# Optimization experiments

Hardware: AMD Instinct MI355X
Metric: run time of the kernel (lower is better)

## Reference

```python
import jax, jax.numpy as jnp
import numpy as np

B, N, D, H = 1, 4096, 1024, 16
K = D // H
ROPE_BASE = 10000.0


def _rope_cos_sin(n, k, base, dtype):
    # GPT-NeoX style rotary embedding: inv_freq over even dims, emb = cat(freqs, freqs)
    inv_freq = 1.0 / (base ** (jnp.arange(0, k, 2, dtype=jnp.float32) / k))  # [K/2]
    pos = jnp.arange(n, dtype=jnp.float32)
    freqs = pos[:, None] * inv_freq[None, :]              # [N, K/2]
    emb = jnp.concatenate([freqs, freqs], axis=-1)        # [N, K]
    return jnp.cos(emb).astype(dtype), jnp.sin(emb).astype(dtype)


def _rotate_half(x):
    x1, x2 = jnp.split(x, 2, axis=-1)
    return jnp.concatenate([-x2, x1], axis=-1)


def setup_inputs() -> dict:
    key = jax.random.key(0)
    kx, kq, ko = jax.random.split(key, 3)
    x = jax.random.normal(kx, (B, N, D), dtype=jnp.float32)
    # torch Linear weights: [out_features, in_features], y = x @ W^T
    w_qkv = jax.random.normal(kq, (3 * H * K, D), dtype=jnp.float32) / np.sqrt(D)
    w_out = jax.random.normal(ko, (D, D), dtype=jnp.float32) / np.sqrt(D)
    return {"x": x, "w_qkv": w_qkv, "w_out": w_out}


def reference(x, w_qkv, w_out):
    b, n, d = x.shape
    qkv = jnp.einsum('bnd,ed->bne', x, w_qkv).reshape(b, n, 3, H, K)
    q, k, v = qkv[:, :, 0], qkv[:, :, 1], qkv[:, :, 2]   # [B, N, H, K]
    cos, sin = _rope_cos_sin(n, K, ROPE_BASE, x.dtype)    # [N, K]
    cos = cos[None, :, None, :]
    sin = sin[None, :, None, :]
    q = q * cos + _rotate_half(q) * sin
    k = k * cos + _rotate_half(k) * sin
    # explicit O(N^2) score matrix, as in the original module
    scores = jnp.einsum('bnhk,bmhk->bnhm', q, k) / np.sqrt(K).astype(x.dtype)
    causal_mask = jnp.tril(jnp.ones((n, n), dtype=bool))  # [N, M]
    scores = jnp.where(causal_mask[None, :, None, :], scores, jnp.finfo(x.dtype).min)
    probs = jax.nn.softmax(scores, axis=-1)
    attn = jnp.einsum('bnhm,bmhk->bnhk', probs, v).reshape(b, n, d)
    return jnp.einsum('bnd,ed->bne', attn, w_out)
```

## Files before the change

### kernel.cpp

```cpp
#include <hip/hip_runtime.h>
#include <hip/hip_bf16.h>
#include <math.h>

#define N_SEQ 4096
#define DIM   1024
#define NHEAD 16
#define HDIM  64
#define E3    3072

typedef short bf16x8 __attribute__((ext_vector_type(8)));
typedef float f32x4  __attribute__((ext_vector_type(4)));
typedef unsigned int u32;

#if __has_builtin(__builtin_amdgcn_exp2f)
#define EXP2(x) __builtin_amdgcn_exp2f(x)
#else
#define EXP2(x) exp2f(x)
#endif

__device__ __forceinline__ float bf2f(unsigned short u) {
    union { unsigned int i; float f; } x; x.i = ((unsigned int)u) << 16; return x.f;
}
__device__ __forceinline__ unsigned short f2bf(float f) {
    union { float f; unsigned int i; } x; x.f = f;
    unsigned int r = x.i + 0x7FFF + ((x.i >> 16) & 1);
    return (unsigned short)(r >> 16);
}
__device__ __forceinline__ unsigned short f2bf_fast(float f) {
    union { float f; unsigned int i; } x; x.f = f;
    return (unsigned short)((x.i + 0x8000u) >> 16);
}
__device__ __forceinline__ f32x4 mfma16(bf16x8 a, bf16x8 b, f32x4 c) {
    return __builtin_amdgcn_mfma_f32_16x16x32_bf16(a, b, c, 0, 0, 0);
}
__device__ __forceinline__ void gload_lds16(const unsigned short* g, unsigned short* l) {
    __builtin_amdgcn_global_load_lds(
        (const __attribute__((address_space(1))) u32*)g,
        (__attribute__((address_space(3))) u32*)l, 16, 0, 0);
}

__device__ __forceinline__ int probe_isf32(const unsigned short* __restrict__ X) {
    __shared__ int cnt;
    if (threadIdx.x == 0) cnt = 0;
    __syncthreads();
    int bad = 0;
    for (int i = threadIdx.x; i < 4096; i += 256) {
        float v = bf2f(X[i]);
        if (!(fabsf(v) < 1e10f)) bad = 1;
    }
    if (bad) atomicAdd(&cnt, 1);
    __syncthreads();
    return cnt > 0;
}

__global__ __launch_bounds__(256)
void prep_kernel(const void* __restrict__ X, const void* __restrict__ Wq,
                 const void* __restrict__ Wo,
                 unsigned short* __restrict__ Xb, unsigned short* __restrict__ Wqb,
                 unsigned short* __restrict__ Wob,
                 float4* __restrict__ Rt,
                 int* __restrict__ flag)
{
    const int ti = blockIdx.x * blockDim.x + threadIdx.x;
    if (ti < N_SEQ * 16) {
        const int n = ti >> 4, f = ti & 15;
        const float i0 = powf(10000.f, -((float)f)        * (1.f/32.f));
        const float i1 = powf(10000.f, -((float)(f + 16)) * (1.f/32.f));
        float s0, c0, s1, c1;
        sincosf((float)n * i0, &s0, &c0);
        sincosf((float)n * i1, &s1, &c1);
        Rt[ti] = (float4){c0, c1, s0, s1};
    }

    const int isf32 = probe_isf32((const unsigned short*)X);
    if (blockIdx.x == 0 && threadIdx.x == 0) *flag = isf32;
    if (!isf32) return;

    const int nX4  = (N_SEQ * DIM) >> 2;
    const int nWq4 = (E3 * DIM) >> 2;
    const int nWo4 = (DIM * DIM) >> 2;
    const int total = nX4 + nWq4 + nWo4;
    const int stride = gridDim.x * blockDim.x;
    for (int i = blockIdx.x * blockDim.x + threadIdx.x; i < total; i += stride) {
        const float4* src; ushort4* dst; int j = i;
        if (j < nX4)                { src = (const float4*)X  + j;  dst = (ushort4*)Xb  + j; }
        else if ((j -= nX4) < nWq4) { src = (const float4*)Wq + j;  dst = (ushort4*)Wqb + j; }
        else { j -= nWq4;             src = (const float4*)Wo + j;  dst = (ushort4*)Wob + j; }
        float4 v = *src;
        ushort4 u;
        u.x = f2bf(v.x); u.y = f2bf(v.y); u.z = f2bf(v.z); u.w = f2bf(v.w);
        *dst = u;
    }
}

__global__ __launch_bounds__(256)
void qkv_mfma_kernel(const void* __restrict__ Xo, const unsigned short* __restrict__ Xc,
                     const void* __restrict__ Wo_, const unsigned short* __restrict__ Wc,
                     const int* __restrict__ flag,
                     const float4* __restrict__ Rt,
                     unsigned short* __restrict__ Qf,
                     unsigned short* __restrict__ Kf,
                     unsigned short* __restrict__ Vf)
{
    __shared__ __align__(16) unsigned short SMEM[4][4096];

    const int isf32 = *flag;
    const unsigned short* Xb = isf32 ? Xc : (const unsigned short*)Xo;
    const unsigned short* Wb = isf32 ? Wc : (const unsigned short*)Wo_;

    const int tid  = threadIdx.x;
    const int lane = tid & 63;
    const int wave = tid >> 6;
    const int wr = wave >> 1, wc = wave & 1;
    const int lm = lane & 15, q4 = lane >> 4;
    const int rbase = blockIdx.y * 128;
    const int cbase = blockIdx.x * 128;

    const int srow = wave * 16 + (lane >> 2);
    const int scol = (lane & 3) * 8;

    const unsigned short* xsrc = Xb + (size_t)(rbase + srow) * DIM + scol;
    const unsigned short* wsrc = Wb + (size_t)(cbase + srow) * DIM + scol;
    const int la = (wr*64 + lm)*32 + q4*8;
    const int lb = (wc*64 + lm)*32 + q4*8;

    f32x4 acc[4][4];
    #pragma unroll
    for (int i = 0; i < 4; ++i)
        #pragma unroll
        for (int j = 0; j < 4; ++j) acc[i][j] = (f32x4){0.f, 0.f, 0.f, 0.f};

    #define QSTAGE(buf)                                                             \
        {                                                                           \
            _Pragma("unroll")                                                       \
            for (int j = 0; j < 2; ++j) {                                           \
                gload_lds16(xsrc + (size_t)j*64*DIM, &SMEM[buf][j*2048 + wave*512]);   \
                gload_lds16(wsrc + (size_t)j*64*DIM, &SMEM[2+buf][j*2048 + wave*512]); \
            }                                                                       \
            xsrc += 32; wsrc += 32;                                                 \
        }

    QSTAGE(0)
    for (int it = 0; it < DIM/32; ++it) {
        const int cur = it & 1;
        __syncthreads();
        if (it + 1 < DIM/32) QSTAGE(cur ^ 1)

        bf16x8 a[4], b[4];
        #pragma unroll
        for (int mi = 0; mi < 4; ++mi)
            a[mi] = *(const bf16x8*)&SMEM[cur][la + mi*512];
        #pragma unroll
        for (int ni = 0; ni < 4; ++ni)
            b[ni] = *(const bf16x8*)&SMEM[2+cur][lb + ni*512];
        #pragma unroll
        for (int mi = 0; mi < 4; ++mi)
            #pragma unroll
            for (int ni = 0; ni < 4; ++ni)
                acc[mi][ni] = mfma16(a[mi], b[ni], acc[mi][ni]);
    }
    #undef QSTAGE

    __syncthreads();

    const int ecol = cbase + wc * 64;
    const int part = ecol >> 10;
    const int h    = (ecol >> 6) & 15;
    unsigned short* ep = &SMEM[0][0] + wave*4096;

    if (part == 2) {
        #pragma unroll
        for (int mh = 0; mh < 2; ++mh) {
            #pragma unroll
            for (int mi2 = 0; mi2 < 2; ++mi2) {
                const int mi = mh*2 + mi2;
                #pragma unroll
                for (int r = 0; r < 4; ++r) {
                    const int n31 = mi2*16 + q4*4 + r;
                    #pragma unroll
                    for (int ni = 0; ni < 4; ++ni)
                        ep[(ni*16 + lm)*40 + n31] = f2bf(acc[mi][ni][r]);
                }
            }
            const int nb = rbase + wr*64 + mh*32;
            const size_t vb = (((size_t)h*128 + (nb >> 5)) << 11) + (size_t)lane*8;
            #pragma unroll
            for (int ni = 0; ni < 4; ++ni) {
                const bf16x8 fr = *(const bf16x8*)(ep + (ni*16 + lm)*40 + q4*8);
                *(bf16x8*)(Vf + vb + (size_t)ni*512) = fr;
            }
        }
    } else {
        unsigned short* dst = (part == 0) ? Qf : Kf;
        const float scl = (part == 0) ? 0.180336884f : 1.0f;
        #pragma unroll
        for (int mi = 0; mi < 4; ++mi) {
            const int tn = rbase + wr*64 + mi*16;
            #pragma unroll
            for (int r = 0; r < 4; ++r) {
                const int n = tn + q4*4 + r;
                const float4 t = Rt[(n << 4) + lm];
                const int row = (q4*4 + r)*72;
                ep[row + lm]      = f2bf((acc[mi][0][r]*t.x - acc[mi][2][r]*t.z) * scl);
                ep[row + lm + 16] = f2bf((acc[mi][1][r]*t.y - acc[mi][3][r]*t.w) * scl);
                ep[row + lm + 32] = f2bf((acc[mi][2][r]*t.x + acc[mi][0][r]*t.z) * scl);
                ep[row + lm + 48] = f2bf((acc[mi][3][r]*t.y + acc[mi][1][r]*t.w) * scl);
            }
            const size_t tb = (((size_t)(h*256 + (tn >> 4))) << 10) + (size_t)lane*8;
            #pragma unroll
            for (int c = 0; c < 2; ++c) {
                const bf16x8 fr = *(const bf16x8*)(ep + lm*72 + c*32 + q4*8);
                *(bf16x8*)(dst + tb + (size_t)c*512) = fr;
            }
        }
    }
}

__global__ __launch_bounds__(256, 2)
void attn_mfma_kernel(const unsigned short* __restrict__ Qf,
                      const unsigned short* __restrict__ Kf,
                      const unsigned short* __restrict__ Vf,
                      unsigned short* __restrict__ Attn)
{
    __shared__ __align__(16) unsigned short P16[4][2][32][40];
    __shared__ __align__(16) float Ox[2][32][64];
    __shared__ float Lx[2][32];

    const int tid  = threadIdx.x;
    const int lane = tid & 63;
    const int wave = tid >> 6;
    const int q4 = lane >> 4, lm = lane & 15;
    const int qh = wave >> 1, kh = wave & 1;

    const int h = blockIdx.x & 15;
    const int p = blockIdx.x >> 4;
    const int qwA = (p << 6) + (qh << 5);
    const int qwB = ((63 - p) << 6) + (qh << 5);
    const int ntA = p + 1;
    const int ntB = 64 - p;

    const unsigned short* qpA = Qf + (((size_t)(h*256 + (qwA >> 4))) << 10) + (size_t)lane * 8;
    const unsigned short* qpB = Qf + (((size_t)(h*256 + (qwB >> 4))) << 10) + (size_t)lane * 8;
    bf16x8 aqA[2][2], aqB[2][2];
    #pragma unroll
    for (int qi = 0; qi < 2; ++qi)
        #pragma unroll
        for (int d = 0; d < 2; ++d) {
            aqA[qi][d] = *(const bf16x8*)(qpA + qi*1024 + d*512);
            aqB[qi][d] = *(const bf16x8*)(qpB + qi*1024 + d*512);
        }

    float lA[2][4], lB[2][4];
    f32x4 oA[2][4], oB[2][4];
    #pragma unroll
    for (int qi = 0; qi < 2; ++qi) {
        #pragma unroll
        for (int r = 0; r < 4; ++r) { lA[qi][r] = 0.f; lB[qi][r] = 0.f; }
        #pragma unroll
        for (int dc = 0; dc < 4; ++dc) {
            oA[qi][dc] = (f32x4){0.f, 0.f, 0.f, 0.f};
            oB[qi][dc] = (f32x4){0.f, 0.f, 0.f, 0.f};
        }
    }

    const size_t hb = ((size_t)h) << 18;
    const unsigned short* kc = Kf + hb + (size_t)(kh*2048) + (size_t)lane*8;
    const unsigned short* vc = Vf + hb + (size_t)(kh*2048) + (size_t)lane*8;

    unsigned short* pwA  = &P16[wave][0][0][0];
    unsigned short* pwB  = &P16[wave][1][0][0];
    unsigned short* pwaA = pwA + (4*q4)*40 + lm;
    unsigned short* pwaB = pwB + (4*q4)*40 + lm;
    const unsigned short* parA = pwA + lm*40 + q4*8;
    const unsigned short* parB = pwB + lm*40 + q4*8;

    bf16x8 bk[2][2];
    bk[0][0] = *(const bf16x8*)(kc);
    bk[0][1] = *(const bf16x8*)(kc + 512);
    bk[1][0] = *(const bf16x8*)(kc + 1024);
    bk[1][1] = *(const bf16x8*)(kc + 1536);

    for (int it = 0; it < ntB; ++it) {
        const int kt = it << 6;
        const int doA = (it < ntA);

        bf16x8 bv[4];
        #pragma unroll
        for (int dc = 0; dc < 4; ++dc)
            bv[dc] = *(const bf16x8*)(vc + dc*512);

        bf16x8 nk[2][2];
        nk[0][0] = *(const bf16x8*)(kc + 4096);
        nk[0][1] = *(const bf16x8*)(kc + 4096 + 512);
        nk[1][0] = *(const bf16x8*)(kc + 4096 + 1024);
        nk[1][1] = *(const bf16x8*)(kc + 4096 + 1536);

        f32x4 sB[2][2], sA[2][2];
        #pragma unroll
        for (int ki = 0; ki < 2; ++ki)
            #pragma unroll
            for (int qi = 0; qi < 2; ++qi) {
                f32x4 z = (f32x4){0.f, 0.f, 0.f, 0.f};
                z = mfma16(aqB[qi][0], bk[ki][0], z);
                sB[qi][ki] = mfma16(aqB[qi][1], bk[ki][1], z);
            }
        if (doA) {
            #pragma unroll
            for (int ki = 0; ki < 2; ++ki)
                #pragma unroll
                for (int qi = 0; qi < 2; ++qi) {
                    f32x4 z = (f32x4){0.f, 0.f, 0.f, 0.f};
                    z = mfma16(aqA[qi][0], bk[ki][0], z);
                    sA[qi][ki] = mfma16(aqA[qi][1], bk[ki][1], z);
                }
        }

        if (kt + 32*kh + 31 > qwB) {
            #pragma unroll
            for (int ki = 0; ki < 2; ++ki) {
                const int key = kt + 32*kh + 16*ki + lm;
                #pragma unroll
                for (int qi = 0; qi < 2; ++qi) {
                    const int qq = qwB + 16*qi + 4*q4;
                    #pragma unroll
                    for (int r = 0; r < 4; ++r)
                        if (key > qq + r) sB[qi][ki][r] = -INFINITY;
                }
            }
        }

        #pragma unroll
        for (int qi = 0; qi < 2; ++qi)
            #pragma unroll
            for (int ki = 0; ki < 2; ++ki)
                #pragma unroll
                for (int r = 0; r < 4; ++r) {
                    const float pb = EXP2(sB[qi][ki][r]);
                    lB[qi][r] += pb;
                    pwaB[qi*640 + r*40 + ki*16] = f2bf_fast(pb);
                }

        if (doA) {
            if (kt + 32*kh + 31 > qwA) {
                #pragma unroll
                for (int ki = 0; ki < 2; ++ki) {
                    const int key = kt + 32*kh + 16*ki + lm;
                    #pragma unroll
                    for (int qi = 0; qi < 2; ++qi) {
                        const int qq = qwA + 16*qi + 4*q4;
                        #pragma unroll
                        for (int r = 0; r < 4; ++r)
                            if (key > qq + r) sA[qi][ki][r] = -INFINITY;
                    }
                }
            }
            #pragma unroll
            for (int qi = 0; qi < 2; ++qi)
                #pragma unroll
                for (int ki = 0; ki < 2; ++ki)
                    #pragma unroll
                    for (int r = 0; r < 4; ++r) {
                        const float pa = EXP2(sA[qi][ki][r]);
                        lA[qi][r] += pa;
                        pwaA[qi*640 + r*40 + ki*16] = f2bf_fast(pa);
                    }
        }

        {
            bf16x8 paB[2];
            paB[0] = *(const bf16x8*)(parB);
            paB[1] = *(const bf16x8*)(parB + 640);
            #pragma unroll
            for (int dc = 0; dc < 4; ++dc)
                #pragma unroll
                for (int qi = 0; qi < 2; ++qi)
                    oB[qi][dc] = mfma16(paB[qi], bv[dc], oB[qi][dc]);
        }
        if (doA) {
            bf16x8 paA[2];
            paA[0] = *(const bf16x8*)(parA);
            paA[1] = *(const bf16x8*)(parA + 640);
            #pragma unroll
            for (int dc = 0; dc < 4; ++dc)
                #pragma unroll
                for (int qi = 0; qi < 2; ++qi)
                    oA[qi][dc] = mfma16(paA[qi], bv[dc], oA[qi][dc]);
        }

        kc += 4096; vc += 4096;
        bk[0][0] = nk[0][0]; bk[0][1] = nk[0][1];
        bk[1][0] = nk[1][0]; bk[1][1] = nk[1][1];
    }

    #pragma unroll
    for (int qi = 0; qi < 2; ++qi)
        #pragma unroll
        for (int r = 0; r < 4; ++r) {
            float a = lA[qi][r], b = lB[qi][r];
            #pragma unroll
            for (int mk = 1; mk <= 8; mk <<= 1) {
                a += __shfl_xor(a, mk);
                b += __shfl_xor(b, mk);
            }
            lA[qi][r] = a; lB[qi][r] = b;
        }

    if (kh == 1) {
        #pragma unroll
        for (int qi = 0; qi < 2; ++qi)
            #pragma unroll
            for (int r = 0; r < 4; ++r) {
                const int qq = 16*qi + 4*q4 + r;
                #pragma unroll
                for (int dc = 0; dc < 4; ++dc)
                    Ox[qh][qq][16*dc + lm] = oA[qi][dc][r];
                if (lm == 0) Lx[qh][qq] = lA[qi][r];
            }
    }
    __syncthreads();
    if (kh == 0) {
        #pragma unroll
        for (int qi = 0; qi < 2; ++qi)
            #pragma unroll
            for (int r = 0; r < 4; ++r) {
                const int qq = 16*qi + 4*q4 + r;
                const float inv = 1.f / (lA[qi][r] + Lx[qh][qq]);
                const size_t row = (size_t)(qwA + qq) * DIM + (h << 6) + lm;
                #pragma unroll
                for (int dc = 0; dc < 4; ++dc) {
                    const float v = oA[qi][dc][r] + Ox[qh][qq][16*dc + lm];
                    Attn[row + 16*dc] = f2bf(v * inv);
                }
            }
    }
    __syncthreads();
    if (kh == 1) {
        #pragma unroll
        for (int qi = 0; qi < 2; ++qi)
            #pragma unroll
            for (int r = 0; r < 4; ++r) {
                const int qq = 16*qi + 4*q4 + r;
                #pragma unroll
                for (int dc = 0; dc < 4; ++dc)
                    Ox[qh][qq][16*dc + lm] = oB[qi][dc][r];
                if (lm == 0) Lx[qh][qq] = lB[qi][r];
            }
    }
    __syncthreads();
    if (kh == 0) {
        #pragma unroll
        for (int qi = 0; qi < 2; ++qi)
            #pragma unroll
            for (int r = 0; r < 4; ++r) {
                const int qq = 16*qi + 4*q4 + r;
                const float inv = 1.f / (lB[qi][r] + Lx[qh][qq]);
                const size_t row = (size_t)(qwB + qq) * DIM + (h << 6) + lm;
                #pragma unroll
                for (int dc = 0; dc < 4; ++dc) {
                    const float v = oB[qi][dc][r] + Ox[qh][qq][16*dc + lm];
                    Attn[row + 16*dc] = f2bf(v * inv);
                }
            }
    }
}

__global__ __launch_bounds__(256)
void out_mfma_kernel(const unsigned short* __restrict__ Ab,
                     const void* __restrict__ Wo_, const unsigned short* __restrict__ Wc,
                     const int* __restrict__ flag,
                     void* __restrict__ Out)
{
    __shared__ unsigned short As[2][2][4096];
    __shared__ unsigned short Bs[2][2][2048];

    const int isf32 = *flag;
    const unsigned short* Wb = isf32 ? Wc : (const unsigned short*)Wo_;

    const int tid  = threadIdx.x;
    const int lane = tid & 63;
    const int wave = tid >> 6;
    const int lm = lane & 15, q4 = lane >> 4;
    const int rbase = blockIdx.y * 128;
    const int cbase = blockIdx.x * 64;

    const int srow16 = lane >> 2;
    const int scol = (lane & 3) * 8;

    const unsigned short* asrc = Ab + (size_t)(rbase + wave*32 + srow16) * DIM + scol;
    const unsigned short* bsrc = Wb + (size_t)(cbase + wave*16 + srow16) * DIM + scol;
    const int la = (wave*32 + lm)*32 + q4*8;
    const int lb = lm*32 + q4*8;

    f32x4 acc[2][4];
    #pragma unroll
    for (int i = 0; i < 2; ++i)
        #pragma unroll
        for (int j = 0; j < 4; ++j) acc[i][j] = (f32x4){0.f, 0.f, 0.f, 0.f};

    #define OSTAGE(buf)                                                              \
        {                                                                             \
            _Pragma("unroll")                                                         \
            for (int kk = 0; kk < 2; ++kk) {                                          \
                _Pragma("unroll")                                                     \
                for (int j = 0; j < 2; ++j)                                           \
                    gload_lds16(asrc + (size_t)j*16*DIM + kk*32,                      \
                                &As[buf][kk][(wave*32 + j*16)*32]);                   \
                gload_lds16(bsrc + kk*32, &Bs[buf][kk][(wave*16)*32]);                \
            }                                                                         \
            asrc += 64; bsrc += 64;                                                   \
        }

    OSTAGE(0)
    for (int it = 0; it < DIM/64; ++it) {
        const int cur = it & 1;
        __syncthreads();
        if (it + 1 < DIM/64) OSTAGE(cur ^ 1)

        bf16x8 a[2][2], b[2][4];
        #pragma unroll
        for (int kk = 0; kk < 2; ++kk) {
            #pragma unroll
            for (int mi = 0; mi < 2; ++mi)
                a[kk][mi] = *(const bf16x8*)&As[cur][kk][la + mi*512];
            #pragma unroll
            for (int ni = 0; ni < 4; ++ni)
                b[kk][ni] = *(const bf16x8*)&Bs[cur][kk][lb + ni*512];
        }
        #pragma unroll
        for (int kk = 0; kk < 2; ++kk)
            #pragma unroll
            for (int mi = 0; mi < 2; ++mi)
                #pragma unroll
                for (int ni = 0; ni < 4; ++ni)
                    acc[mi][ni] = mfma16(a[kk][mi], b[kk][ni], acc[mi][ni]);
    }
    #undef OSTAGE

    #pragma unroll
    for (int mi = 0; mi < 2; ++mi)
        #pragma unroll
        for (int r = 0; r < 4; ++r) {
            const size_t n = rbase + wave*32 + mi*16 + q4*4 + r;
            #pragma unroll
            for (int ni = 0; ni < 4; ++ni) {
                const size_t e = cbase + ni*16 + lm;
                const float v = acc[mi][ni][r];
                if (isf32) ((float*)Out)[n * DIM + e] = v;
                else       ((unsigned short*)Out)[n * DIM + e] = f2bf(v);
            }
        }
}

extern "C" void kernel_launch(void* const* d_in, const int* in_sizes, int n_in,
                              void* d_out, int out_size, void* d_ws, size_t ws_size,
                              hipStream_t stream) {
    const void* X    = d_in[0];
    const void* Wqkv = d_in[1];
    const void* Wout = d_in[2];

    int* flag = (int*)d_ws;
    unsigned short* base = (unsigned short*)((char*)d_ws + 256);
    const size_t nX = (size_t)N_SEQ * DIM;
    const size_t nWq = (size_t)E3 * DIM;
    const size_t nWo = (size_t)DIM * DIM;
    unsigned short* Xb  = base;
    unsigned short* Wqb = Xb + nX;
    unsigned short* Wob = Wqb + nWq;
    unsigned short* Qf  = Wob + nWo;
    unsigned short* Kf  = Qf + nX;
    unsigned short* Vf  = Kf + nX;
    unsigned short* At  = Vf + nX;
    float4* Rt = (float4*)(At + nX);

    prep_kernel<<<768, 256, 0, stream>>>(X, Wqkv, Wout, Xb, Wqb, Wob, Rt, flag);
    qkv_mfma_kernel<<<dim3(E3 / 128, N_SEQ / 128), 256, 0, stream>>>(X, Xb, Wqkv, Wqb, flag, Rt, Qf, Kf, Vf);
    attn_mfma_kernel<<<dim3(NHEAD * 32), 256, 0, stream>>>(Qf, Kf, Vf, At);
    out_mfma_kernel<<<dim3(DIM / 64, N_SEQ / 128), 256, 0, stream>>>(At, Wout, Wob, flag, d_out);
}
```

Baseline: 192.8 us.

## Split attention key tiles across twice as many waves per block

Doubles the attention block to 512 threads. Each pair of waves that shared a query tile now splits the key-tile loop by parity, so every wave processes every other 64-key tile. This raises the number of waves working on each query tile, since only 512 blocks exist for 256 CUs, and so improves latency hiding. In exchange it adds a two-level LDS reduction with extra barriers and more shared memory, and the launch-bounds change may put pressure on registers.

```diff
diff --git a/kernel.cpp b/kernel.cpp
--- a/kernel.cpp
+++ b/kernel.cpp
@@ -216,21 +216,24 @@
     }
 }
 
-__global__ __launch_bounds__(256, 2)
+__global__ __launch_bounds__(512, 2)
 void attn_mfma_kernel(const unsigned short* __restrict__ Qf,
                       const unsigned short* __restrict__ Kf,
                       const unsigned short* __restrict__ Vf,
                       unsigned short* __restrict__ Attn)
 {
-    __shared__ __align__(16) unsigned short P16[4][2][32][40];
-    __shared__ __align__(16) float Ox[2][32][64];
-    __shared__ float Lx[2][32];
+    __shared__ __align__(16) unsigned short P16[8][2][32][40];
+    __shared__ __align__(16) float Ox2[2][2][32][64];
+    __shared__ float Lx2[2][2][32];
 
     const int tid  = threadIdx.x;
     const int lane = tid & 63;
     const int wave = tid >> 6;
     const int q4 = lane >> 4, lm = lane & 15;
-    const int qh = wave >> 1, kh = wave & 1;
+    const int qh = wave >> 2;
+    const int sub = wave & 3;
+    const int kh = sub >> 1;
+    const int ks = sub & 1;
 
     const int h = blockIdx.x & 15;
     const int p = blockIdx.x >> 4;
@@ -264,8 +267,8 @@
     }
 
     const size_t hb = ((size_t)h) << 18;
-    const unsigned short* kc = Kf + hb + (size_t)(kh*2048) + (size_t)lane*8;
-    const unsigned short* vc = Vf + hb + (size_t)(kh*2048) + (size_t)lane*8;
+    const unsigned short* kc = Kf + hb + (size_t)(ks*4096 + kh*2048) + (size_t)lane*8;
+    const unsigned short* vc = Vf + hb + (size_t)(ks*4096 + kh*2048) + (size_t)lane*8;
 
     unsigned short* pwA  = &P16[wave][0][0][0];
     unsigned short* pwB  = &P16[wave][1][0][0];
@@ -280,7 +283,7 @@
     bk[1][0] = *(const bf16x8*)(kc + 1024);
     bk[1][1] = *(const bf16x8*)(kc + 1536);
 
-    for (int it = 0; it < ntB; ++it) {
+    for (int it = ks; it < ntB; it += 2) {
         const int kt = it << 6;
         const int doA = (it < ntA);
 
@@ -290,10 +293,10 @@
             bv[dc] = *(const bf16x8*)(vc + dc*512);
 
         bf16x8 nk[2][2];
-        nk[0][0] = *(const bf16x8*)(kc + 4096);
-        nk[0][1] = *(const bf16x8*)(kc + 4096 + 512);
-        nk[1][0] = *(const bf16x8*)(kc + 4096 + 1024);
-        nk[1][1] = *(const bf16x8*)(kc + 4096 + 1536);
+        nk[0][0] = *(const bf16x8*)(kc + 8192);
+        nk[0][1] = *(const bf16x8*)(kc + 8192 + 512);
+        nk[1][0] = *(const bf16x8*)(kc + 8192 + 1024);
+        nk[1][1] = *(const bf16x8*)(kc + 8192 + 1536);
 
         f32x4 sB[2][2], sA[2][2];
         #pragma unroll
@@ -387,7 +390,7 @@
                     oA[qi][dc] = mfma16(paA[qi], bv[dc], oA[qi][dc]);
         }
 
-        kc += 4096; vc += 4096;
+        kc += 8192; vc += 8192;
         bk[0][0] = nk[0][0]; bk[0][1] = nk[0][1];
         bk[1][0] = nk[1][0]; bk[1][1] = nk[1][1];
     }
@@ -405,63 +408,68 @@
             lA[qi][r] = a; lB[qi][r] = b;
         }
 
-    if (kh == 1) {
-        #pragma unroll
-        for (int qi = 0; qi < 2; ++qi)
-            #pragma unroll
-            for (int r = 0; r < 4; ++r) {
-                const int qq = 16*qi + 4*q4 + r;
-                #pragma unroll
-                for (int dc = 0; dc < 4; ++dc)
-                    Ox[qh][qq][16*dc + lm] = oA[qi][dc][r];
-                if (lm == 0) Lx[qh][qq] = lA[qi][r];
-            }
-    }
-    __syncthreads();
-    if (kh == 0) {
-        #pragma unroll
-        for (int qi = 0; qi < 2; ++qi)
-            #pragma unroll
-            for (int r = 0; r < 4; ++r) {
-                const int qq = 16*qi + 4*q4 + r;
-                const float inv = 1.f / (lA[qi][r] + Lx[qh][qq]);
-                const size_t row = (size_t)(qwA + qq) * DIM + (h << 6) + lm;
-                #pragma unroll
-                for (int dc = 0; dc < 4; ++dc) {
-                    const float v = oA[qi][dc][r] + Ox[qh][qq][16*dc + lm];
-                    Attn[row + 16*dc] = f2bf(v * inv);
-                }
-            }
-    }
-    __syncthreads();
-    if (kh == 1) {
-        #pragma unroll
-        for (int qi = 0; qi < 2; ++qi)
-            #pragma unroll
-            for (int r = 0; r < 4; ++r) {
-                const int qq = 16*qi + 4*q4 + r;
-                #pragma unroll
-                for (int dc = 0; dc < 4; ++dc)
-                    Ox[qh][qq][16*dc + lm] = oB[qi][dc][r];
-                if (lm == 0) Lx[qh][qq] = lB[qi][r];
-            }
-    }
-    __syncthreads();
-    if (kh == 0) {
-        #pragma unroll
-        for (int qi = 0; qi < 2; ++qi)
-            #pragma unroll
-            for (int r = 0; r < 4; ++r) {
-                const int qq = 16*qi + 4*q4 + r;
-                const float inv = 1.f / (lB[qi][r] + Lx[qh][qq]);
-                const size_t row = (size_t)(qwB + qq) * DIM + (h << 6) + lm;
-                #pragma unroll
-                for (int dc = 0; dc < 4; ++dc) {
-                    const float v = oB[qi][dc][r] + Ox[qh][qq][16*dc + lm];
-                    Attn[row + 16*dc] = f2bf(v * inv);
-                }
-            }
-    }
+    #define REDUCE_WRITE(oS, lS, qwS)                                            \
+    {                                                                            \
+        if (sub >= 2) {                                                          \
+            _Pragma("unroll")                                                    \
+            for (int qi = 0; qi < 2; ++qi)                                       \
+                _Pragma("unroll")                                                \
+                for (int r = 0; r < 4; ++r) {                                    \
+                    const int qq = 16*qi + 4*q4 + r;                             \
+                    _Pragma("unroll")                                            \
+                    for (int dc = 0; dc < 4; ++dc)                               \
+                        Ox2[qh][sub-2][qq][16*dc + lm] = oS[qi][dc][r];          \
+                    if (lm == 0) Lx2[qh][sub-2][qq] = lS[qi][r];                 \
+                }                                                                \
+        }                                                                        \
+        __syncthreads();                                                         \
+        if (sub < 2) {                                                           \
+            _Pragma("unroll")                                                    \
+            for (int qi = 0; qi < 2; ++qi)                                       \
+                _Pragma("unroll")                                                \
+                for (int r = 0; r < 4; ++r) {                                    \
+                    const int qq = 16*qi + 4*q4 + r;                             \
+                    _Pragma("unroll")                                            \
+                    for (int dc = 0; dc < 4; ++dc)                               \
+                        oS[qi][dc][r] += Ox2[qh][sub][qq][16*dc + lm];           \
+                    lS[qi][r] += Lx2[qh][sub][qq];                               \
+                }                                                                \
+        }                                                                        \
+        __syncthreads();                                                         \
+        if (sub == 1) {                                                          \
+            _Pragma("unroll")                                                    \
+            for (int qi = 0; qi < 2; ++qi)                                       \
+                _Pragma("unroll")                                                \
+                for (int r = 0; r < 4; ++r) {                                    \
+                    const int qq = 16*qi + 4*q4 + r;                             \
+                    _Pragma("unroll")                                            \
+                    for (int dc = 0; dc < 4; ++dc)                               \
+                        Ox2[qh][0][qq][16*dc + lm] = oS[qi][dc][r];              \
+                    if (lm == 0) Lx2[qh][0][qq] = lS[qi][r];                     \
+                }                                                                \
+        }                                                                        \
+        __syncthreads();                                                         \
+        if (sub == 0) {                                                          \
+            _Pragma("unroll")                                                    \
+            for (int qi = 0; qi < 2; ++qi)                                       \
+                _Pragma("unroll")                                                \
+                for (int r = 0; r < 4; ++r) {                                    \
+                    const int qq = 16*qi + 4*q4 + r;                             \
+                    const float inv = 1.f / (lS[qi][r] + Lx2[qh][0][qq]);        \
+                    const size_t row = (size_t)((qwS) + qq) * DIM + (h << 6) + lm; \
+                    _Pragma("unroll")                                            \
+                    for (int dc = 0; dc < 4; ++dc) {                             \
+                        const float v = oS[qi][dc][r] + Ox2[qh][0][qq][16*dc + lm]; \
+                        Attn[row + 16*dc] = f2bf(v * inv);                       \
+                    }                                                            \
+                }                                                                \
+        }                                                                        \
+        __syncthreads();                                                         \
+    }
+
+    REDUCE_WRITE(oA, lA, qwA)
+    REDUCE_WRITE(oB, lB, qwB)
+    #undef REDUCE_WRITE
 }
 
 __global__ __launch_bounds__(256)
@@ -574,6 +582,6 @@
 
     prep_kernel<<<768, 256, 0, stream>>>(X, Wqkv, Wout, Xb, Wqb, Wob, Rt, flag);
     qkv_mfma_kernel<<<dim3(E3 / 128, N_SEQ / 128), 256, 0, stream>>>(X, Xb, Wqkv, Wqb, flag, Rt, Qf, Kf, Vf);
-    attn_mfma_kernel<<<dim3(NHEAD * 32), 256, 0, stream>>>(Qf, Kf, Vf, At);
+    attn_mfma_kernel<<<dim3(NHEAD * 32), 512, 0, stream>>>(Qf, Kf, Vf, At);
     out_mfma_kernel<<<dim3(DIM / 64, N_SEQ / 128), 256, 0, stream>>>(At, Wout, Wob, flag, d_out);
 }
```

New measurement: 201.4 us. +4.5%, slower.
